# Kernel optimization log

Measured on AMD Instinct MI355X. Metric: run time of the kernel, lower is better.

## Reference

```python
import jax, jax.numpy as jnp
import numpy as np


def setup_inputs() -> dict:
    key = jax.random.key(0)
    k1, k2, k3 = jax.random.split(key, 3)
    B, N, D, YD = 128, 500000, 64, 1
    return {
        "x": jax.random.normal(k1, (B, D), dtype=jnp.float32),
        "pool_x": jax.random.normal(k2, (N, D), dtype=jnp.float32),
        "pool_y": jax.random.normal(k3, (N, YD), dtype=jnp.float32),
        "size_retrieval_set": 10,
    }


def reference(x, pool_x, pool_y, size_retrieval_set):
    # Euclidean cdist via the expanded quadratic form (same math as torch.cdist p=2).
    x_sq = jnp.sum(x * x, axis=-1, keepdims=True)            # [B, 1]
    p_sq = jnp.sum(pool_x * pool_x, axis=-1)                 # [N]
    cross = jnp.einsum("bd,nd->bn", x, pool_x)               # [B, N]
    dist = jnp.sqrt(jnp.maximum(x_sq + p_sq[None, :] - 2.0 * cross, 0.0))  # [B, N]
    # ascending sort + take first k  ==  top_k of negated distances
    _, indices = jax.lax.top_k(-dist, size_retrieval_set)    # [B, k]
    # gather + concat: [B, k, x_dim + y_dim]
    retrieval_set = jnp.concatenate([pool_x[indices], pool_y[indices]], axis=-1)
    return retrieval_set
```

## Files before the change

### kernel.cpp

```cpp
#include <hip/hip_runtime.h>
#include <hip/hip_bf16.h>
#include <cfloat>
#include <climits>

typedef short  short8v __attribute__((ext_vector_type(8)));
typedef float  f32x4   __attribute__((ext_vector_type(4)));

#define NQ    128
#define SR    16
#define SPB   8
#define RPB   (SR * SPB)
#define EMIT  3
#define K2    6
#define KSEL  24
#define KK    10

__device__ __forceinline__ bool pair_less(float d1, int i1, float d2, int i2) {
    return (d1 < d2) || (d1 == d2 && i1 < i2);
}

__device__ __forceinline__ unsigned pk2(float a, float b) {
    union { __hip_bfloat162 h; unsigned u; } cv;
    cv.h = __float22bfloat162_rn(make_float2(a, b));
    return cv.u;
}
__device__ __forceinline__ short8v pack8(float4 a, float4 b) {
    union { unsigned u[4]; short8v s; } cv;
    cv.u[0] = pk2(a.x, a.y); cv.u[1] = pk2(a.z, a.w);
    cv.u[2] = pk2(b.x, b.y); cv.u[3] = pk2(b.z, b.w);
    return cv.s;
}

__device__ __forceinline__ void ins2(float (&d)[2], int (&ix)[2], float key, int idx) {
    if (!(key < d[1])) return;
    d[1] = key; ix[1] = idx;
    bool sw = d[1] < d[0];
    float a = d[0], b = d[1]; int ai = ix[0], bi2 = ix[1];
    d[0] = sw ? b : a; ix[0] = sw ? bi2 : ai;
    d[1] = sw ? a : b; ix[1] = sw ? ai : bi2;
}

__device__ __forceinline__ void ins3p(float (&d)[3], int (&ix)[3], float key, int idx) {
    if (!pair_less(key, idx, d[2], ix[2])) return;
    d[2] = key; ix[2] = idx;
#pragma unroll
    for (int j = 2; j > 0; --j) {
        float a = d[j - 1], b = d[j]; int ai = ix[j - 1], bi2 = ix[j];
        bool sw = pair_less(b, bi2, a, ai);
        d[j - 1] = sw ? b : a; ix[j - 1] = sw ? bi2 : ai;
        d[j]     = sw ? a : b; ix[j]     = sw ? ai : bi2;
    }
}

__device__ __forceinline__ void ins6(float (&d)[K2], int (&ix)[K2], float key, int idx) {
    if (!pair_less(key, idx, d[K2 - 1], ix[K2 - 1])) return;
    d[K2 - 1] = key; ix[K2 - 1] = idx;
#pragma unroll
    for (int j = K2 - 1; j > 0; --j) {
        float a = d[j - 1], b = d[j]; int ai = ix[j - 1], bi2 = ix[j];
        bool sw = pair_less(b, bi2, a, ai);
        d[j - 1] = sw ? b : a; ix[j - 1] = sw ? bi2 : ai;
        d[j]     = sw ? a : b; ix[j]     = sw ? ai : bi2;
    }
}

__device__ __forceinline__ void argmin64(float& k, int& i, int& l) {
#pragma unroll
    for (int off = 32; off; off >>= 1) {
        float ok = __shfl_xor(k, off);
        int   oi = __shfl_xor(i, off);
        int   ol = __shfl_xor(l, off);
        bool take = pair_less(ok, oi, k, i) || (ok == k && oi == i && ol < l);
        k = take ? ok : k; i = take ? oi : i; l = take ? ol : l;
    }
}

__global__ __launch_bounds__(64, 3) void phase1(
        const float* __restrict__ x, const float* __restrict__ pool_x,
        float2* __restrict__ cand, int N, int nblocks) {
    const int lane = threadIdx.x;
    const int c = lane & 15, g = lane >> 4;
    const int blk = blockIdx.x;
    const long brow = (long)blk * RPB;

    short8v bfrag[8][2];
#pragma unroll
    for (int tt = 0; tt < 8; ++tt)
#pragma unroll
        for (int ks = 0; ks < 2; ++ks) {
            const float* xp = x + (tt * 16 + c) * 64 + ks * 32 + g * 8;
            float4 u0 = *(const float4*)xp;
            float4 u1 = *(const float4*)(xp + 4);
            u0.x *= -2.f; u0.y *= -2.f; u0.z *= -2.f; u0.w *= -2.f;
            u1.x *= -2.f; u1.y *= -2.f; u1.z *= -2.f; u1.w *= -2.f;
            bfrag[tt][ks] = pack8(u0, u1);
        }

    float bd[8][2]; int bi[8][2];
#pragma unroll
    for (int tt = 0; tt < 8; ++tt) {
        bd[tt][0] = FLT_MAX; bd[tt][1] = FLT_MAX;
        bi[tt][0] = INT_MAX; bi[tt][1] = INT_MAX;
    }

    float4 nf0, nf1, nf2, nf3;
    auto LOADS = [&](int s) {
        long r = brow + (long)s * SR + c;
        if (r > (long)N - 1) r = (long)N - 1;
        const float* pr = pool_x + r * 64 + g * 8;
        nf0 = *(const float4*)pr;
        nf1 = *(const float4*)(pr + 4);
        nf2 = *(const float4*)(pr + 32);
        nf3 = *(const float4*)(pr + 36);
    };
    LOADS(0);

#pragma unroll
    for (int s = 0; s < SPB; ++s) {
        float4 f0 = nf0, f1 = nf1, f2 = nf2, f3 = nf3;
        if (s + 1 < SPB) LOADS(s + 1);

        float ps = f0.x * f0.x + f0.y * f0.y + f0.z * f0.z + f0.w * f0.w
                 + f1.x * f1.x + f1.y * f1.y + f1.z * f1.z + f1.w * f1.w
                 + f2.x * f2.x + f2.y * f2.y + f2.z * f2.z + f2.w * f2.w
                 + f3.x * f3.x + f3.y * f3.y + f3.z * f3.z + f3.w * f3.w;
        ps += __shfl_xor(ps, 16);
        ps += __shfl_xor(ps, 32);
        if (brow + (long)s * SR + c >= N) ps = __builtin_inff();

        f32x4 psqv;
#pragma unroll
        for (int r = 0; r < 4; ++r) psqv[r] = __shfl(ps, g * 4 + r);

        short8v a0 = pack8(f0, f1);
        short8v a1 = pack8(f2, f3);
        const int rowb = (int)brow + s * SR + g * 4;

#pragma unroll
        for (int tt = 0; tt < 8; ++tt) {
            f32x4 acc = __builtin_amdgcn_mfma_f32_16x16x32_bf16(a0, bfrag[tt][0], psqv, 0, 0, 0);
            acc = __builtin_amdgcn_mfma_f32_16x16x32_bf16(a1, bfrag[tt][1], acc, 0, 0, 0);
            float mn = fminf(fminf(acc[0], acc[1]), fminf(acc[2], acc[3]));
            if (mn < bd[tt][1]) {
#pragma unroll
                for (int r = 0; r < 4; ++r) ins2(bd[tt], bi[tt], acc[r], rowb + r);
            }
        }
    }

#pragma unroll
    for (int tt = 0; tt < 8; ++tt) {
        float md[3] = {bd[tt][0], bd[tt][1], FLT_MAX};
        int   mi[3] = {bi[tt][0], bi[tt][1], INT_MAX};
#pragma unroll
        for (int m = 16; m <= 32; m <<= 1) {
            float od[3]; int oi[3];
#pragma unroll
            for (int j = 0; j < 3; ++j) { od[j] = __shfl_xor(md[j], m); oi[j] = __shfl_xor(mi[j], m); }
#pragma unroll
            for (int j = 0; j < 3; ++j) ins3p(md, mi, od[j], oi[j]);
        }
        if (g < 3) {
            int q = tt * 16 + c;
            cand[(size_t)q * nblocks * EMIT + blk * EMIT + g] =
                make_float2(md[g], __int_as_float(mi[g]));
        }
    }
}

__global__ __launch_bounds__(256) void phase2(
        const float2* __restrict__ cand, const float* __restrict__ x,
        const float* __restrict__ pool_x, const float* __restrict__ pool_y,
        float* __restrict__ out, int nblocks, int N) {
    __shared__ float xs[64];
    __shared__ float wd[4 * KSEL]; __shared__ int wi[4 * KSEL];
    __shared__ float sd[KSEL];     __shared__ int si[KSEL];
    __shared__ float rk[64];
    __shared__ int   fi[KK];

    const int t = threadIdx.x, wave = t >> 6, lane = t & 63;
    const int q = blockIdx.x;
    if (t < 64) xs[t] = x[q * 64 + t];

    const int M = nblocks * EMIT;
    float d[K2]; int ix[K2];
#pragma unroll
    for (int j = 0; j < K2; ++j) { d[j] = FLT_MAX; ix[j] = INT_MAX; }

    const float2* cq = cand + (size_t)q * M;
    for (int m = t; m < M; m += 256) {
        float2 e = cq[m];
        ins6(d, ix, e.x, __float_as_int(e.y));
    }

    for (int r = 0; r < KSEL; ++r) {
        float mk = d[0]; int mi = ix[0]; int ml = lane;
        argmin64(mk, mi, ml);
        if (lane == ml) {
#pragma unroll
            for (int j = 0; j < K2 - 1; ++j) { d[j] = d[j + 1]; ix[j] = ix[j + 1]; }
            d[K2 - 1] = FLT_MAX; ix[K2 - 1] = INT_MAX;
        }
        if (lane == 0) { wd[wave * KSEL + r] = mk; wi[wave * KSEL + r] = mi; }
    }
    __syncthreads();

    if (wave == 0) {
        float e0 = wd[lane]; int e0i = wi[lane];
        float e1 = (lane + 64 < 4 * KSEL) ? wd[lane + 64] : FLT_MAX;
        int  e1i = (lane + 64 < 4 * KSEL) ? wi[lane + 64] : INT_MAX;
        if (pair_less(e1, e1i, e0, e0i)) {
            float tf = e0; e0 = e1; e1 = tf;
            int   ti = e0i; e0i = e1i; e1i = ti;
        }
        for (int r = 0; r < KSEL; ++r) {
            float mk = e0; int mi = e0i; int ml = lane;
            argmin64(mk, mi, ml);
            if (lane == ml) { e0 = e1; e0i = e1i; e1 = FLT_MAX; e1i = INT_MAX; }
            if (lane == 0) { sd[r] = mk; si[r] = mi; }
        }
    }
    __syncthreads();

    if (t < 64) {
        float key = FLT_MAX;
        if (t < KSEL) {
            int idx = si[t];
            if (idx >= 0 && idx < N) {
                const float4* pr = (const float4*)(pool_x + (size_t)idx * 64);
                const float4* xv = (const float4*)xs;
                float psq = 0.f, dot = 0.f;
#pragma unroll
                for (int k4 = 0; k4 < 16; ++k4) {
                    float4 p = pr[k4]; float4 xw = xv[k4];
                    psq += p.x * p.x + p.y * p.y + p.z * p.z + p.w * p.w;
                    dot += p.x * xw.x + p.y * xw.y + p.z * xw.z + p.w * xw.w;
                }
                key = psq - 2.0f * dot;
            }
        }
        rk[t] = key;
    }
    __syncthreads();

    if (wave == 0) {
        float mykey = rk[lane];
        int myidx = (lane < KSEL) ? si[lane] : INT_MAX;
        for (int r = 0; r < KK; ++r) {
            float mk = mykey; int mi = myidx; int ml = lane;
            argmin64(mk, mi, ml);
            if (lane == ml) { mykey = FLT_MAX; myidx = INT_MAX; }
            if (lane == 0) fi[r] = mi;
        }
    }
    __syncthreads();

    for (int e = t; e < KK * 65; e += 256) {
        int j = e / 65, cdim = e - j * 65;
        int idx = fi[j];
        out[(size_t)q * (KK * 65) + e] = (cdim < 64) ? pool_x[(size_t)idx * 64 + cdim]
                                                     : pool_y[idx];
    }
}

extern "C" void kernel_launch(void* const* d_in, const int* in_sizes, int n_in,
                              void* d_out, int out_size, void* d_ws, size_t ws_size,
                              hipStream_t stream) {
    const float* x      = (const float*)d_in[0];
    const float* pool_x = (const float*)d_in[1];
    const float* pool_y = (const float*)d_in[2];
    const int N = in_sizes[1] / 64;

    const int nblocks = (N + RPB - 1) / RPB;

    float2* cand = (float2*)d_ws;

    hipLaunchKernelGGL(phase1, dim3(nblocks), dim3(64), 0, stream,
                       x, pool_x, cand, N, nblocks);
    hipLaunchKernelGGL(phase2, dim3(NQ), dim3(256), 0, stream,
                       cand, x, pool_x, pool_y, (float*)d_out, nblocks, N);
}
```

Before: 304.3 us.

## Split queries across waves in 256-thread blocks and fold pool norms via MFMA

Phase1 now runs four waves per block. Each wave handles 64 of the 128 queries and one of two row chunks, which halves the per-wave query fragments and running-best registers so more waves can be resident. The pool-row squared norm is injected into the accumulator with an extra bf16 MFMA against a one-hot operand, replacing the cross-lane shuffles. The norm is therefore rounded to bf16, which may perturb tie or near-tie ordering. Each pool row is now loaded twice (once per query half), and the candidate layout becomes chunk-major, with phase2 reading it accordingly.

```diff
diff --git a/kernel.cpp b/kernel.cpp
--- a/kernel.cpp
+++ b/kernel.cpp
@@ -8,8 +8,8 @@
 
 #define NQ    128
 #define SR    16
-#define SPB   8
-#define RPB   (SR * SPB)
+#define SPW   8
+#define RPC   (SR * SPW)
 #define EMIT  3
 #define K2    6
 #define KSEL  24
@@ -75,20 +75,21 @@
     }
 }
 
-__global__ __launch_bounds__(64, 3) void phase1(
+__global__ __launch_bounds__(256, 4) void phase1(
         const float* __restrict__ x, const float* __restrict__ pool_x,
-        float2* __restrict__ cand, int N, int nblocks) {
-    const int lane = threadIdx.x;
+        float2* __restrict__ cand, int N, int nchunks) {
+    const int t = threadIdx.x, wv = t >> 6, lane = t & 63;
     const int c = lane & 15, g = lane >> 4;
-    const int blk = blockIdx.x;
-    const long brow = (long)blk * RPB;
-
-    short8v bfrag[8][2];
-#pragma unroll
-    for (int tt = 0; tt < 8; ++tt)
+    const int qbase = (wv >> 1) * 64;
+    const int chunk = blockIdx.x * 2 + (wv & 1);
+    const long brow = (long)chunk * RPC;
+
+    short8v bfrag[4][2];
+#pragma unroll
+    for (int tt = 0; tt < 4; ++tt)
 #pragma unroll
         for (int ks = 0; ks < 2; ++ks) {
-            const float* xp = x + (tt * 16 + c) * 64 + ks * 32 + g * 8;
+            const float* xp = x + (qbase + tt * 16 + c) * 64 + ks * 32 + g * 8;
             float4 u0 = *(const float4*)xp;
             float4 u1 = *(const float4*)(xp + 4);
             u0.x *= -2.f; u0.y *= -2.f; u0.z *= -2.f; u0.w *= -2.f;
@@ -96,49 +97,54 @@
             bfrag[tt][ks] = pack8(u0, u1);
         }
 
-    float bd[8][2]; int bi[8][2];
-#pragma unroll
-    for (int tt = 0; tt < 8; ++tt) {
+    short8v b2 = {0, 0, 0, 0, 0, 0, 0, 0};
+    b2[0] = (short)0x3F80;
+
+    float bd[4][2]; int bi[4][2];
+#pragma unroll
+    for (int tt = 0; tt < 4; ++tt) {
         bd[tt][0] = FLT_MAX; bd[tt][1] = FLT_MAX;
         bi[tt][0] = INT_MAX; bi[tt][1] = INT_MAX;
     }
 
-    float4 nf0, nf1, nf2, nf3;
-    auto LOADS = [&](int s) {
+    float4 buf[2][4];
+    auto LOAD = [&](int s, int b) {
         long r = brow + (long)s * SR + c;
         if (r > (long)N - 1) r = (long)N - 1;
         const float* pr = pool_x + r * 64 + g * 8;
-        nf0 = *(const float4*)pr;
-        nf1 = *(const float4*)(pr + 4);
-        nf2 = *(const float4*)(pr + 32);
-        nf3 = *(const float4*)(pr + 36);
+        buf[b][0] = *(const float4*)pr;
+        buf[b][1] = *(const float4*)(pr + 4);
+        buf[b][2] = *(const float4*)(pr + 32);
+        buf[b][3] = *(const float4*)(pr + 36);
     };
-    LOADS(0);
-
-#pragma unroll
-    for (int s = 0; s < SPB; ++s) {
-        float4 f0 = nf0, f1 = nf1, f2 = nf2, f3 = nf3;
-        if (s + 1 < SPB) LOADS(s + 1);
+    LOAD(0, 0);
+
+#pragma unroll
+    for (int s = 0; s < SPW; ++s) {
+        const int b = s & 1;
+        if (s + 1 < SPW) LOAD(s + 1, b ^ 1);
+        float4 f0 = buf[b][0], f1 = buf[b][1], f2 = buf[b][2], f3 = buf[b][3];
 
         float ps = f0.x * f0.x + f0.y * f0.y + f0.z * f0.z + f0.w * f0.w
                  + f1.x * f1.x + f1.y * f1.y + f1.z * f1.z + f1.w * f1.w
                  + f2.x * f2.x + f2.y * f2.y + f2.z * f2.z + f2.w * f2.w
                  + f3.x * f3.x + f3.y * f3.y + f3.z * f3.z + f3.w * f3.w;
-        ps += __shfl_xor(ps, 16);
-        ps += __shfl_xor(ps, 32);
         if (brow + (long)s * SR + c >= N) ps = __builtin_inff();
 
-        f32x4 psqv;
-#pragma unroll
-        for (int r = 0; r < 4; ++r) psqv[r] = __shfl(ps, g * 4 + r);
+        short8v a2 = {0, 0, 0, 0, 0, 0, 0, 0};
+        union { unsigned u; short s2[2]; } pv; pv.u = pk2(ps, 0.f);
+        a2[0] = pv.s2[0];
 
         short8v a0 = pack8(f0, f1);
         short8v a1 = pack8(f2, f3);
+
+        f32x4 zc = {0.f, 0.f, 0.f, 0.f};
+        f32x4 pacc = __builtin_amdgcn_mfma_f32_16x16x32_bf16(a2, b2, zc, 0, 0, 0);
+
         const int rowb = (int)brow + s * SR + g * 4;
-
-#pragma unroll
-        for (int tt = 0; tt < 8; ++tt) {
-            f32x4 acc = __builtin_amdgcn_mfma_f32_16x16x32_bf16(a0, bfrag[tt][0], psqv, 0, 0, 0);
+#pragma unroll
+        for (int tt = 0; tt < 4; ++tt) {
+            f32x4 acc = __builtin_amdgcn_mfma_f32_16x16x32_bf16(a0, bfrag[tt][0], pacc, 0, 0, 0);
             acc = __builtin_amdgcn_mfma_f32_16x16x32_bf16(a1, bfrag[tt][1], acc, 0, 0, 0);
             float mn = fminf(fminf(acc[0], acc[1]), fminf(acc[2], acc[3]));
             if (mn < bd[tt][1]) {
@@ -149,7 +155,7 @@
     }
 
 #pragma unroll
-    for (int tt = 0; tt < 8; ++tt) {
+    for (int tt = 0; tt < 4; ++tt) {
         float md[3] = {bd[tt][0], bd[tt][1], FLT_MAX};
         int   mi[3] = {bi[tt][0], bi[tt][1], INT_MAX};
 #pragma unroll
@@ -161,8 +167,8 @@
             for (int j = 0; j < 3; ++j) ins3p(md, mi, od[j], oi[j]);
         }
         if (g < 3) {
-            int q = tt * 16 + c;
-            cand[(size_t)q * nblocks * EMIT + blk * EMIT + g] =
+            int q = qbase + tt * 16 + c;
+            cand[((size_t)chunk * NQ + q) * EMIT + g] =
                 make_float2(md[g], __int_as_float(mi[g]));
         }
     }
@@ -171,7 +177,7 @@
 __global__ __launch_bounds__(256) void phase2(
         const float2* __restrict__ cand, const float* __restrict__ x,
         const float* __restrict__ pool_x, const float* __restrict__ pool_y,
-        float* __restrict__ out, int nblocks, int N) {
+        float* __restrict__ out, int nchunks, int N) {
     __shared__ float xs[64];
     __shared__ float wd[4 * KSEL]; __shared__ int wi[4 * KSEL];
     __shared__ float sd[KSEL];     __shared__ int si[KSEL];
@@ -182,15 +188,17 @@
     const int q = blockIdx.x;
     if (t < 64) xs[t] = x[q * 64 + t];
 
-    const int M = nblocks * EMIT;
     float d[K2]; int ix[K2];
 #pragma unroll
     for (int j = 0; j < K2; ++j) { d[j] = FLT_MAX; ix[j] = INT_MAX; }
 
-    const float2* cq = cand + (size_t)q * M;
-    for (int m = t; m < M; m += 256) {
-        float2 e = cq[m];
-        ins6(d, ix, e.x, __float_as_int(e.y));
+    for (int ch = t; ch < nchunks; ch += 256) {
+        const float2* e = cand + ((size_t)ch * NQ + q) * EMIT;
+#pragma unroll
+        for (int g2 = 0; g2 < EMIT; ++g2) {
+            float2 v = e[g2];
+            ins6(d, ix, v.x, __float_as_int(v.y));
+        }
     }
 
     for (int r = 0; r < KSEL; ++r) {
@@ -271,12 +279,13 @@
     const float* pool_y = (const float*)d_in[2];
     const int N = in_sizes[1] / 64;
 
-    const int nblocks = (N + RPB - 1) / RPB;
+    const int nblocks = (N + 2 * RPC - 1) / (2 * RPC);
+    const int nchunks = nblocks * 2;
 
     float2* cand = (float2*)d_ws;
 
-    hipLaunchKernelGGL(phase1, dim3(nblocks), dim3(64), 0, stream,
-                       x, pool_x, cand, N, nblocks);
+    hipLaunchKernelGGL(phase1, dim3(nblocks), dim3(256), 0, stream,
+                       x, pool_x, cand, N, nchunks);
     hipLaunchKernelGGL(phase2, dim3(NQ), dim3(256), 0, stream,
-                       cand, x, pool_x, pool_y, (float*)d_out, nblocks, N);
-}
+                       cand, x, pool_x, pool_y, (float*)d_out, nchunks, N);
+}
```

Result: faster. 258.1 us (-15.2%).
